# Kernel optimization log

Hardware: AMD Instinct MI355X
Metric: run time of the kernel (lower is better)

## Reference

```python
import jax, jax.numpy as jnp
import numpy as np
import math

D_MODEL = 1024
N_HEADS = 16
D_HEAD = D_MODEL // N_HEADS
DECAY_MAX = 0.99  # buggy torch init: only the LAST head's decay rate survives the loop
LN_EPS = 1e-5


def setup_inputs() -> dict:
    key = jax.random.key(0)
    ks = jax.random.split(key, 12)
    B, S = 2, 2048
    x = jax.random.normal(ks[0], (B, S, D_MODEL), dtype=jnp.float32)
    def w(k):
        return jax.random.normal(k, (D_MODEL, D_MODEL), dtype=jnp.float32) * 0.02
    return {
        "x": x,
        "Wq": w(ks[1]), "bq": jnp.zeros((D_MODEL,), jnp.float32),
        "Wk": w(ks[2]), "bk": jnp.zeros((D_MODEL,), jnp.float32),
        "Wv": w(ks[3]), "bv": jnp.zeros((D_MODEL,), jnp.float32),
        "Wg": w(ks[4]), "bg": jnp.zeros((D_MODEL,), jnp.float32),
        "Wo": w(ks[5]), "bo": jnp.zeros((D_MODEL,), jnp.float32),
        "gamma": jnp.ones((D_MODEL,), jnp.float32),
        "beta": jnp.zeros((D_MODEL,), jnp.float32),
    }


def _decay_mask(S):
    # faithful to torch buffer: decay_matrix[i,j] = DECAY_MAX**(i-j) for j<=i else 0
    i = jnp.arange(S, dtype=jnp.float32)[:, None]
    j = jnp.arange(S, dtype=jnp.float32)[None, :]
    diff = i - j
    return jnp.where(diff >= 0, jnp.power(jnp.float32(DECAY_MAX), diff), 0.0)  # [S,S]


def reference(x, Wq, bq, Wk, bk, Wv, bv, Wg, bg, Wo, bo, gamma, beta):
    B, S, D = x.shape
    H, DH = N_HEADS, D_HEAD
    # projections -> [B,H,S,DH]
    Q = (x @ Wq + bq).reshape(B, S, H, DH).transpose(0, 2, 1, 3)
    K = (x @ Wk + bk).reshape(B, S, H, DH).transpose(0, 2, 1, 3)
    V = (x @ Wv + bv).reshape(B, S, H, DH).transpose(0, 2, 1, 3)
    scores = jnp.einsum('bhsd,bhtd->bhst', Q, K) / math.sqrt(DH)  # [B,H,S,S]
    mask = _decay_mask(S)  # [S,S], broadcast over B,H (head-independent per torch bug)
    retained = jnp.einsum('bhst,bhtd->bhsd', scores * mask, V)
    retained = retained.transpose(0, 2, 1, 3).reshape(B, S, D)
    # LayerNorm over last dim
    mu = jnp.mean(retained, axis=-1, keepdims=True)
    var = jnp.var(retained, axis=-1, keepdims=True)
    normed = (retained - mu) * jax.lax.rsqrt(var + LN_EPS) * gamma + beta
    G = jax.nn.sigmoid(x @ Wg + bg)
    return (normed * G) @ Wo + bo  # dropout = identity (eval)
```

## Files before the change

### kernel.cpp

```cpp
#include <hip/hip_runtime.h>

typedef __attribute__((ext_vector_type(4))) float f32x4;
typedef __attribute__((ext_vector_type(8))) short bf16x8;
typedef unsigned short USHORT;

static __device__ __forceinline__ float bf2f(USHORT u) {
    return __uint_as_float(((unsigned)u) << 16);
}
static __device__ __forceinline__ USHORT f2bf(float f) {
    unsigned u = __float_as_uint(f);
    unsigned r = u + 0x7FFF + ((u >> 16) & 1);
    return (USHORT)(r >> 16);
}

#define GLDS16(gp, lp) __builtin_amdgcn_global_load_lds(                      \
    (const __attribute__((address_space(1))) unsigned int*)(gp),              \
    (__attribute__((address_space(3))) unsigned int*)(lp), 16, 0, 0)

__global__ __launch_bounds__(256) void k_cast_x(const float* __restrict__ x,
                                                USHORT* __restrict__ xb) {
    const int i = (blockIdx.x * 256 + threadIdx.x) * 4;
    float4 v = *(const float4*)&x[i];
    *(ushort4*)&xb[i] = make_ushort4(f2bf(v.x), f2bf(v.y), f2bf(v.z), f2bf(v.w));
}

struct TWArgs { const float* src[5]; USHORT* dst[5]; };

__global__ __launch_bounds__(256) void k_transpose_w(TWArgs ta) {
    const float* __restrict__ W  = ta.src[blockIdx.z];
    USHORT* __restrict__      WT = ta.dst[blockIdx.z];
    __shared__ USHORT t[64][65];
    const int k0 = blockIdx.y * 64, n0 = blockIdx.x * 64;
    const int tid = threadIdx.x;
#pragma unroll
    for (int s = 0; s < 4; s++) {
        int slot = tid + s * 256;
        int row = slot >> 4, c4 = (slot & 15) * 4;
        float4 vv = *(const float4*)&W[(size_t)(k0 + row) * 1024 + n0 + c4];
        t[row][c4 + 0] = f2bf(vv.x);
        t[row][c4 + 1] = f2bf(vv.y);
        t[row][c4 + 2] = f2bf(vv.z);
        t[row][c4 + 3] = f2bf(vv.w);
    }
    __syncthreads();
#pragma unroll
    for (int s = 0; s < 2; s++) {
        int slot = tid + s * 256;
        int n = slot >> 3, c8 = (slot & 7) * 8;
        USHORT tmp[8];
#pragma unroll
        for (int u = 0; u < 8; u++) tmp[u] = t[c8 + u][n];
        *(int4*)&WT[(size_t)(n0 + n) * 1024 + k0 + c8] = *(int4*)tmp;
    }
}

struct GArgs {
    const USHORT* A;
    const USHORT* W[4];
    const float*  bias[4];
    void*         dst[4];
    USHORT*       dstv;
    float         scale[4];
    int           mode[4];
};

__global__ __launch_bounds__(256, 2) void k_gemm(GArgs ga) {
    const int z = blockIdx.z;
    const USHORT* __restrict__ A  = ga.A;
    const USHORT* __restrict__ BT = ga.W[z];
    __shared__ USHORT As[128 * 32];
    __shared__ USHORT Bs[128 * 32];
    const int tid = threadIdx.x;
    const int m0 = blockIdx.y * 128, n0 = blockIdx.x * 128;
    const int w = tid >> 6, l = tid & 63, lr = l & 15, q = l >> 4;
    const int wr = w >> 1, wc = w & 1;
    const int srow = tid >> 2, sco = (tid & 3) * 8;
    f32x4 acc[4][4] = {};
    for (int k0 = 0; k0 < 1024; k0 += 32) {
        __syncthreads();
        GLDS16(&A [(size_t)(m0 + srow)      * 1024 + k0 + sco], &As[srow * 32 + sco]);
        GLDS16(&A [(size_t)(m0 + srow + 64) * 1024 + k0 + sco], &As[(srow + 64) * 32 + sco]);
        GLDS16(&BT[(size_t)(n0 + srow)      * 1024 + k0 + sco], &Bs[srow * 32 + sco]);
        GLDS16(&BT[(size_t)(n0 + srow + 64) * 1024 + k0 + sco], &Bs[(srow + 64) * 32 + sco]);
        __syncthreads();
        bf16x8 af[4], bfr[4];
#pragma unroll
        for (int mi = 0; mi < 4; mi++)
            af[mi] = *(const bf16x8*)&As[(wr * 64 + mi * 16 + lr) * 32 + q * 8];
#pragma unroll
        for (int ni = 0; ni < 4; ni++)
            bfr[ni] = *(const bf16x8*)&Bs[(wc * 64 + ni * 16 + lr) * 32 + q * 8];
#pragma unroll
        for (int mi = 0; mi < 4; mi++)
#pragma unroll
            for (int ni = 0; ni < 4; ni++)
                acc[mi][ni] = __builtin_amdgcn_mfma_f32_16x16x32_bf16(
                    af[mi], bfr[ni], acc[mi][ni], 0, 0, 0);
    }
    const float scale = ga.scale[z];
    const int mode = ga.mode[z];
    const float* __restrict__ bias = ga.bias[z];
#pragma unroll
    for (int ni = 0; ni < 4; ni++) {
        int col = n0 + wc * 64 + ni * 16 + lr;
        float bv = bias[col];
#pragma unroll
        for (int mi = 0; mi < 4; mi++) {
            int r0 = m0 + wr * 64 + mi * 16 + q * 4;
            float vr[4];
#pragma unroll
            for (int r = 0; r < 4; r++) {
                float v = acc[mi][ni][r] + bv;
                if (mode == 1) v = 1.0f / (1.0f + __expf(-v));
                vr[r] = v * scale;
            }
            if (mode == 3) {
                float* df = (float*)ga.dst[z];
#pragma unroll
                for (int r = 0; r < 4; r++)
                    df[(size_t)(r0 + r) * 1024 + col] = vr[r];
            } else if (mode == 2) {
                int b = r0 >> 11, s = r0 & 2047;
                int h = col >> 6, d = col & 63;
                const float NP1 = 1.0101010101010102f;
                float c0 = exp2f(0.014499569695115089f * (float)(s & 63));
                float c1 = c0 * NP1, c2 = c1 * NP1, c3 = c2 * NP1;
                *(ushort4*)&ga.dstv[(size_t)(((b * 16 + h) * 64) + d) * 2048 + s] =
                    make_ushort4(f2bf(vr[0] * c0), f2bf(vr[1] * c1),
                                 f2bf(vr[2] * c2), f2bf(vr[3] * c3));
            } else {
                USHORT* db = (USHORT*)ga.dst[z];
#pragma unroll
                for (int r = 0; r < 4; r++)
                    db[(size_t)(r0 + r) * 1024 + col] = f2bf(vr[r]);
            }
        }
    }
}

__global__ __launch_bounds__(256, 2) void k_attn(const USHORT* __restrict__ Q,
                                                 const USHORT* __restrict__ K,
                                                 const USHORT* __restrict__ VT,
                                                 float* __restrict__ R) {
    const int bh = blockIdx.x;
    const int b = bh >> 4, h = bh & 15;
    const int rr = blockIdx.y;
    const int iblk = (rr < 8) ? rr : 23 - rr;
    const int i0 = iblk * 128;
    const int tid = threadIdx.x, w = tid >> 6, l = tid & 63, lr = l & 15, q = l >> 4;
    __shared__ USHORT Qs[128 * 72];
    __shared__ USHORT Ks[64 * 72];
    __shared__ USHORT Vs[64 * 72];
    __shared__ USHORT Ps[4][32 * 72];
    const float L2D = -0.014499569695115089f;
    const float C16 = 0.8514577710948755f;
#pragma unroll
    for (int s = 0; s < 4; s++) {
        int slot = tid + s * 256;
        int rw = slot >> 3, c8 = (slot & 7) * 8;
        *(int4*)&Qs[rw * 72 + c8] =
            *(const int4*)&Q[(size_t)(b * 2048 + i0 + rw) * 1024 + h * 64 + c8];
    }
    const int iw0 = i0 + w * 32;
    f32x4 accr[4][2] = {};
    const int njb = 2 * iblk + 2;
    for (int jb = 0; jb < njb; jb++) {
        const int j0 = jb * 64;
        {
            int r0_ = tid >> 3, c0 = (tid & 7) * 8;
            int slot1 = tid + 256;
            int r1_ = slot1 >> 3, c1 = (slot1 & 7) * 8;
            int4 kv0 = *(const int4*)&K[(size_t)(b * 2048 + j0 + r0_) * 1024 + h * 64 + c0];
            int4 kv1 = *(const int4*)&K[(size_t)(b * 2048 + j0 + r1_) * 1024 + h * 64 + c1];
            int4 vv0 = *(const int4*)&VT[(size_t)(bh * 64 + r0_) * 2048 + j0 + c0];
            int4 vv1 = *(const int4*)&VT[(size_t)(bh * 64 + r1_) * 2048 + j0 + c1];
            __syncthreads();
            *(int4*)&Ks[r0_ * 72 + c0] = kv0;
            *(int4*)&Ks[r1_ * 72 + c1] = kv1;
            *(int4*)&Vs[r0_ * 72 + c0] = vv0;
            *(int4*)&Vs[r1_ * 72 + c1] = vv1;
            __syncthreads();
        }
        if (j0 <= iw0 + 31) {
            f32x4 accp[4][2] = {};
#pragma unroll
            for (int kk = 0; kk < 2; kk++) {
                bf16x8 bqf[2];
#pragma unroll
                for (int it = 0; it < 2; it++)
                    bqf[it] = *(const bf16x8*)&Qs[(w * 32 + it * 16 + lr) * 72 + kk * 32 + q * 8];
#pragma unroll
                for (int jt = 0; jt < 4; jt++) {
                    bf16x8 akf = *(const bf16x8*)&Ks[(jt * 16 + lr) * 72 + kk * 32 + q * 8];
#pragma unroll
                    for (int it = 0; it < 2; it++)
                        accp[jt][it] = __builtin_amdgcn_mfma_f32_16x16x32_bf16(
                            akf, bqf[it], accp[jt][it], 0, 0, 0);
                }
            }
            const float fb = exp2f(L2D * (float)(iw0 - j0 + lr));
            const float F[2] = { fb, fb * C16 };
            const bool partial = (j0 + 63 > iw0);
#pragma unroll
            for (int jt = 0; jt < 4; jt++) {
#pragma unroll
                for (int it = 0; it < 2; it++) {
                    float v0 = accp[jt][it][0] * F[it];
                    float v1 = accp[jt][it][1] * F[it];
                    float v2 = accp[jt][it][2] * F[it];
                    float v3 = accp[jt][it][3] * F[it];
                    if (partial) {
                        const int ii = iw0 + it * 16 + lr;
                        const int jj = j0 + jt * 16 + q * 4;
                        if (jj + 0 > ii) v0 = 0.0f;
                        if (jj + 1 > ii) v1 = 0.0f;
                        if (jj + 2 > ii) v2 = 0.0f;
                        if (jj + 3 > ii) v3 = 0.0f;
                    }
                    unsigned w0 = __builtin_amdgcn_perm(
                        __float_as_uint(v1), __float_as_uint(v0), 0x07060302u);
                    unsigned w1 = __builtin_amdgcn_perm(
                        __float_as_uint(v3), __float_as_uint(v2), 0x07060302u);
                    *(uint2*)&Ps[w][(it * 16 + lr) * 72 + jt * 16 + q * 4] =
                        make_uint2(w0, w1);
                }
            }
            asm volatile("s_waitcnt lgkmcnt(0)" ::: "memory");
#pragma unroll
            for (int kk = 0; kk < 2; kk++) {
                bf16x8 bpf[2];
#pragma unroll
                for (int it = 0; it < 2; it++)
                    bpf[it] = *(const bf16x8*)&Ps[w][(it * 16 + lr) * 72 + kk * 32 + q * 8];
#pragma unroll
                for (int dt = 0; dt < 4; dt++) {
                    bf16x8 avf = *(const bf16x8*)&Vs[(dt * 16 + lr) * 72 + kk * 32 + q * 8];
#pragma unroll
                    for (int it = 0; it < 2; it++)
                        accr[dt][it] = __builtin_amdgcn_mfma_f32_16x16x32_bf16(
                            avf, bpf[it], accr[dt][it], 0, 0, 0);
                }
            }
        }
    }
#pragma unroll
    for (int it = 0; it < 2; it++) {
        int i = i0 + w * 32 + it * 16 + lr;
#pragma unroll
        for (int dt = 0; dt < 4; dt++) {
            *(f32x4*)&R[(size_t)(b * 2048 + i) * 1024 + h * 64 + dt * 16 + q * 4] =
                accr[dt][it];
        }
    }
}

__global__ __launch_bounds__(256) void k_ln_gate(const float* __restrict__ R,
                                                 const USHORT* __restrict__ G,
                                                 const float* __restrict__ gamma,
                                                 const float* __restrict__ beta,
                                                 USHORT* __restrict__ NG) {
    const int row = blockIdx.x, tid = threadIdx.x;
    const float4 v = *(const float4*)&R[(size_t)row * 1024 + tid * 4];
    float vv[4] = { v.x, v.y, v.z, v.w };
    float s  = vv[0] + vv[1] + vv[2] + vv[3];
    float s2 = vv[0]*vv[0] + vv[1]*vv[1] + vv[2]*vv[2] + vv[3]*vv[3];
#pragma unroll
    for (int o = 32; o > 0; o >>= 1) {
        s  += __shfl_down(s, o, 64);
        s2 += __shfl_down(s2, o, 64);
    }
    __shared__ float red[8];
    if ((tid & 63) == 0) { red[tid >> 6] = s; red[4 + (tid >> 6)] = s2; }
    __syncthreads();
    const float ts  = red[0] + red[1] + red[2] + red[3];
    const float ts2 = red[4] + red[5] + red[6] + red[7];
    const float mu  = ts * (1.0f / 1024.0f);
    const float var = ts2 * (1.0f / 1024.0f) - mu * mu;
    const float inv = rsqrtf(var + 1e-5f);
    ushort4 g4 = *(const ushort4*)&G[(size_t)row * 1024 + tid * 4];
    float4 gm = *(const float4*)&gamma[tid * 4];
    float4 bt = *(const float4*)&beta[tid * 4];
    USHORT gg[4]  = { g4.x, g4.y, g4.z, g4.w };
    float  gmm[4] = { gm.x, gm.y, gm.z, gm.w };
    float  btt[4] = { bt.x, bt.y, bt.z, bt.w };
    USHORT o4[4];
#pragma unroll
    for (int u = 0; u < 4; u++) {
        float nv = (vv[u] - mu) * inv * gmm[u] + btt[u];
        o4[u] = f2bf(nv * bf2f(gg[u]));
    }
    *(ushort4*)&NG[(size_t)row * 1024 + tid * 4] = make_ushort4(o4[0], o4[1], o4[2], o4[3]);
}

extern "C" void kernel_launch(void* const* d_in, const int* in_sizes, int n_in,
                              void* d_out, int out_size, void* d_ws, size_t ws_size,
                              hipStream_t stream) {
    const float* x     = (const float*)d_in[0];
    const float* Wq    = (const float*)d_in[1];
    const float* bq    = (const float*)d_in[2];
    const float* Wk    = (const float*)d_in[3];
    const float* bk    = (const float*)d_in[4];
    const float* Wv    = (const float*)d_in[5];
    const float* bv    = (const float*)d_in[6];
    const float* Wg    = (const float*)d_in[7];
    const float* bg    = (const float*)d_in[8];
    const float* Wo    = (const float*)d_in[9];
    const float* bo    = (const float*)d_in[10];
    const float* gamma = (const float*)d_in[11];
    const float* beta  = (const float*)d_in[12];

    char* ws = (char*)d_ws;
    const size_t MB = 1 << 20;
    USHORT* WqT = (USHORT*)(ws + 0 * MB);
    USHORT* WkT = (USHORT*)(ws + 2 * MB);
    USHORT* WvT = (USHORT*)(ws + 4 * MB);
    USHORT* WgT = (USHORT*)(ws + 6 * MB);
    USHORT* WoT = (USHORT*)(ws + 8 * MB);
    USHORT* Qb  = (USHORT*)(ws + 10 * MB);
    USHORT* Kb  = (USHORT*)(ws + 18 * MB);
    USHORT* VTb = (USHORT*)(ws + 26 * MB);
    USHORT* Gb  = (USHORT*)(ws + 34 * MB);
    USHORT* NGb = Qb;
    USHORT* Xb  = (USHORT*)d_out;
    float*  Rf  = (float*)d_out;

    k_cast_x<<<4096, 256, 0, stream>>>(x, Xb);
    {
        TWArgs ta;
        ta.src[0] = Wq; ta.src[1] = Wk; ta.src[2] = Wv; ta.src[3] = Wg; ta.src[4] = Wo;
        ta.dst[0] = WqT; ta.dst[1] = WkT; ta.dst[2] = WvT; ta.dst[3] = WgT; ta.dst[4] = WoT;
        k_transpose_w<<<dim3(16, 16, 5), 256, 0, stream>>>(ta);
    }
    {
        GArgs ga;
        ga.A = Xb;
        ga.W[0] = WqT; ga.W[1] = WkT; ga.W[2] = WvT; ga.W[3] = WgT;
        ga.bias[0] = bq; ga.bias[1] = bk; ga.bias[2] = bv; ga.bias[3] = bg;
        ga.dst[0] = Qb; ga.dst[1] = Kb; ga.dst[2] = nullptr; ga.dst[3] = Gb;
        ga.dstv = VTb;
        ga.scale[0] = 0.125f; ga.scale[1] = 1.0f; ga.scale[2] = 1.0f; ga.scale[3] = 1.0f;
        ga.mode[0] = 0; ga.mode[1] = 0; ga.mode[2] = 2; ga.mode[3] = 1;
        k_gemm<<<dim3(8, 32, 4), 256, 0, stream>>>(ga);
    }
    k_attn<<<dim3(32, 16), 256, 0, stream>>>(Qb, Kb, VTb, Rf);
    k_ln_gate<<<4096, 256, 0, stream>>>(Rf, Gb, gamma, beta, NGb);
    {
        GArgs go;
        go.A = NGb;
        for (int i = 0; i < 4; i++) {
            go.W[i] = WoT; go.bias[i] = bo; go.dst[i] = d_out;
            go.scale[i] = 1.0f; go.mode[i] = 3;
        }
        go.dstv = nullptr;
        k_gemm<<<dim3(8, 32, 1), 256, 0, stream>>>(go);
    }
}
```

Baseline: 233.6 us.

## Double-buffer LDS tiles in GEMM and attention kernels to overlap loads

The GEMM kernel now holds two LDS buffers for the A/B tiles and issues global-to-LDS loads for the next k-step before computing on the current one, so each iteration needs one barrier instead of two. The attention kernel likewise double-buffers its K/V tiles: it prefetches the next block into registers before computing and writes them into the alternate LDS buffer after compute. The aim is to hide global memory latency behind MFMA work. The cost is doubled LDS use for these tiles, which can lower occupancy, plus extra live registers in attention.

```diff
diff --git a/kernel.cpp b/kernel.cpp
--- a/kernel.cpp
+++ b/kernel.cpp
@@ -16,6 +16,9 @@
 #define GLDS16(gp, lp) __builtin_amdgcn_global_load_lds(                      \
     (const __attribute__((address_space(1))) unsigned int*)(gp),              \
     (__attribute__((address_space(3))) unsigned int*)(lp), 16, 0, 0)
+
+#define LGKM_BARRIER() asm volatile("s_waitcnt lgkmcnt(0)\ns_barrier" ::: "memory")
+#define FULL_BARRIER() asm volatile("s_waitcnt vmcnt(0) lgkmcnt(0)\ns_barrier" ::: "memory")
 
 __global__ __launch_bounds__(256) void k_cast_x(const float* __restrict__ x,
                                                 USHORT* __restrict__ xb) {
@@ -68,28 +71,36 @@
     const int z = blockIdx.z;
     const USHORT* __restrict__ A  = ga.A;
     const USHORT* __restrict__ BT = ga.W[z];
-    __shared__ USHORT As[128 * 32];
-    __shared__ USHORT Bs[128 * 32];
+    __shared__ USHORT As[2][128 * 32];
+    __shared__ USHORT Bs[2][128 * 32];
     const int tid = threadIdx.x;
     const int m0 = blockIdx.y * 128, n0 = blockIdx.x * 128;
     const int w = tid >> 6, l = tid & 63, lr = l & 15, q = l >> 4;
     const int wr = w >> 1, wc = w & 1;
     const int srow = tid >> 2, sco = (tid & 3) * 8;
     f32x4 acc[4][4] = {};
-    for (int k0 = 0; k0 < 1024; k0 += 32) {
-        __syncthreads();
-        GLDS16(&A [(size_t)(m0 + srow)      * 1024 + k0 + sco], &As[srow * 32 + sco]);
-        GLDS16(&A [(size_t)(m0 + srow + 64) * 1024 + k0 + sco], &As[(srow + 64) * 32 + sco]);
-        GLDS16(&BT[(size_t)(n0 + srow)      * 1024 + k0 + sco], &Bs[srow * 32 + sco]);
-        GLDS16(&BT[(size_t)(n0 + srow + 64) * 1024 + k0 + sco], &Bs[(srow + 64) * 32 + sco]);
-        __syncthreads();
+    GLDS16(&A [(size_t)(m0 + srow)      * 1024 + sco], &As[0][srow * 32 + sco]);
+    GLDS16(&A [(size_t)(m0 + srow + 64) * 1024 + sco], &As[0][(srow + 64) * 32 + sco]);
+    GLDS16(&BT[(size_t)(n0 + srow)      * 1024 + sco], &Bs[0][srow * 32 + sco]);
+    GLDS16(&BT[(size_t)(n0 + srow + 64) * 1024 + sco], &Bs[0][(srow + 64) * 32 + sco]);
+    for (int kt = 0; kt < 32; kt++) {
+        const int cur = kt & 1;
+        FULL_BARRIER();
+        if (kt + 1 < 32) {
+            const int k1 = (kt + 1) * 32;
+            const int nxt = 1 - cur;
+            GLDS16(&A [(size_t)(m0 + srow)      * 1024 + k1 + sco], &As[nxt][srow * 32 + sco]);
+            GLDS16(&A [(size_t)(m0 + srow + 64) * 1024 + k1 + sco], &As[nxt][(srow + 64) * 32 + sco]);
+            GLDS16(&BT[(size_t)(n0 + srow)      * 1024 + k1 + sco], &Bs[nxt][srow * 32 + sco]);
+            GLDS16(&BT[(size_t)(n0 + srow + 64) * 1024 + k1 + sco], &Bs[nxt][(srow + 64) * 32 + sco]);
+        }
         bf16x8 af[4], bfr[4];
 #pragma unroll
         for (int mi = 0; mi < 4; mi++)
-            af[mi] = *(const bf16x8*)&As[(wr * 64 + mi * 16 + lr) * 32 + q * 8];
+            af[mi] = *(const bf16x8*)&As[cur][(wr * 64 + mi * 16 + lr) * 32 + q * 8];
 #pragma unroll
         for (int ni = 0; ni < 4; ni++)
-            bfr[ni] = *(const bf16x8*)&Bs[(wc * 64 + ni * 16 + lr) * 32 + q * 8];
+            bfr[ni] = *(const bf16x8*)&Bs[cur][(wc * 64 + ni * 16 + lr) * 32 + q * 8];
 #pragma unroll
         for (int mi = 0; mi < 4; mi++)
 #pragma unroll
@@ -149,8 +160,8 @@
     const int i0 = iblk * 128;
     const int tid = threadIdx.x, w = tid >> 6, l = tid & 63, lr = l & 15, q = l >> 4;
     __shared__ USHORT Qs[128 * 72];
-    __shared__ USHORT Ks[64 * 72];
-    __shared__ USHORT Vs[64 * 72];
+    __shared__ USHORT Ks[2][64 * 72];
+    __shared__ USHORT Vs[2][64 * 72];
     __shared__ USHORT Ps[4][32 * 72];
     const float L2D = -0.014499569695115089f;
     const float C16 = 0.8514577710948755f;
@@ -162,25 +173,29 @@
             *(const int4*)&Q[(size_t)(b * 2048 + i0 + rw) * 1024 + h * 64 + c8];
     }
     const int iw0 = i0 + w * 32;
+    const int r0_ = tid >> 3, c0 = (tid & 7) * 8;
+    const int njb = 2 * iblk + 2;
+    int4 kv0, kv1, vv0, vv1;
+    kv0 = *(const int4*)&K [(size_t)(b * 2048 + r0_)      * 1024 + h * 64 + c0];
+    kv1 = *(const int4*)&K [(size_t)(b * 2048 + r0_ + 32) * 1024 + h * 64 + c0];
+    vv0 = *(const int4*)&VT[(size_t)(bh * 64 + r0_)      * 2048 + c0];
+    vv1 = *(const int4*)&VT[(size_t)(bh * 64 + r0_ + 32) * 2048 + c0];
+    *(int4*)&Ks[0][r0_ * 72 + c0]        = kv0;
+    *(int4*)&Ks[0][(r0_ + 32) * 72 + c0] = kv1;
+    *(int4*)&Vs[0][r0_ * 72 + c0]        = vv0;
+    *(int4*)&Vs[0][(r0_ + 32) * 72 + c0] = vv1;
     f32x4 accr[4][2] = {};
-    const int njb = 2 * iblk + 2;
     for (int jb = 0; jb < njb; jb++) {
         const int j0 = jb * 64;
-        {
-            int r0_ = tid >> 3, c0 = (tid & 7) * 8;
-            int slot1 = tid + 256;
-            int r1_ = slot1 >> 3, c1 = (slot1 & 7) * 8;
-            int4 kv0 = *(const int4*)&K[(size_t)(b * 2048 + j0 + r0_) * 1024 + h * 64 + c0];
-            int4 kv1 = *(const int4*)&K[(size_t)(b * 2048 + j0 + r1_) * 1024 + h * 64 + c1];
-            int4 vv0 = *(const int4*)&VT[(size_t)(bh * 64 + r0_) * 2048 + j0 + c0];
-            int4 vv1 = *(const int4*)&VT[(size_t)(bh * 64 + r1_) * 2048 + j0 + c1];
-            __syncthreads();
-            *(int4*)&Ks[r0_ * 72 + c0] = kv0;
-            *(int4*)&Ks[r1_ * 72 + c1] = kv1;
-            *(int4*)&Vs[r0_ * 72 + c0] = vv0;
-            *(int4*)&Vs[r1_ * 72 + c1] = vv1;
-            __syncthreads();
-        }
+        const int cur = jb & 1;
+        if (jb + 1 < njb) {
+            const int j1 = j0 + 64;
+            kv0 = *(const int4*)&K [(size_t)(b * 2048 + j1 + r0_)      * 1024 + h * 64 + c0];
+            kv1 = *(const int4*)&K [(size_t)(b * 2048 + j1 + r0_ + 32) * 1024 + h * 64 + c0];
+            vv0 = *(const int4*)&VT[(size_t)(bh * 64 + r0_)      * 2048 + j1 + c0];
+            vv1 = *(const int4*)&VT[(size_t)(bh * 64 + r0_ + 32) * 2048 + j1 + c0];
+        }
+        LGKM_BARRIER();
         if (j0 <= iw0 + 31) {
             f32x4 accp[4][2] = {};
 #pragma unroll
@@ -191,7 +206,7 @@
                     bqf[it] = *(const bf16x8*)&Qs[(w * 32 + it * 16 + lr) * 72 + kk * 32 + q * 8];
 #pragma unroll
                 for (int jt = 0; jt < 4; jt++) {
-                    bf16x8 akf = *(const bf16x8*)&Ks[(jt * 16 + lr) * 72 + kk * 32 + q * 8];
+                    bf16x8 akf = *(const bf16x8*)&Ks[cur][(jt * 16 + lr) * 72 + kk * 32 + q * 8];
 #pragma unroll
                     for (int it = 0; it < 2; it++)
                         accp[jt][it] = __builtin_amdgcn_mfma_f32_16x16x32_bf16(
@@ -234,13 +249,20 @@
                     bpf[it] = *(const bf16x8*)&Ps[w][(it * 16 + lr) * 72 + kk * 32 + q * 8];
 #pragma unroll
                 for (int dt = 0; dt < 4; dt++) {
-                    bf16x8 avf = *(const bf16x8*)&Vs[(dt * 16 + lr) * 72 + kk * 32 + q * 8];
+                    bf16x8 avf = *(const bf16x8*)&Vs[cur][(dt * 16 + lr) * 72 + kk * 32 + q * 8];
 #pragma unroll
                     for (int it = 0; it < 2; it++)
                         accr[dt][it] = __builtin_amdgcn_mfma_f32_16x16x32_bf16(
                             avf, bpf[it], accr[dt][it], 0, 0, 0);
                 }
             }
+        }
+        if (jb + 1 < njb) {
+            const int nxt = 1 - cur;
+            *(int4*)&Ks[nxt][r0_ * 72 + c0]        = kv0;
+            *(int4*)&Ks[nxt][(r0_ + 32) * 72 + c0] = kv1;
+            *(int4*)&Vs[nxt][r0_ * 72 + c0]        = vv0;
+            *(int4*)&Vs[nxt][(r0_ + 32) * 72 + c0] = vv1;
         }
     }
 #pragma unroll
```

Result: faster. 225.9 us (-3.3%).

## Replace quadratic decay attention with chunked recurrent form and fuse LayerNorm into output GEMM

Applied to the files above, without the earlier changes.

The full masked S×S attention is replaced with a chunkwise retention formulation. One kernel computes a per-64-row chunk V^T K state, and an apply kernel combines a decayed prefix sum of those states with the intra-chunk causal attention, using a hi/lo bf16 split to keep precision. LayerNorm row statistics are accumulated with atomics in the apply kernel, and normalization plus gating are fused into the A-tile staging of the output GEMM, which removes the separate LN kernel and the fp32 R round trip. The GEMM gains LDS double buffering, and the x cast and weight transpose are merged into one prep launch. In exchange the apply kernel does a serial O(c) prefix reduction over chunk states, and the LN path adds float atomics plus extra per-tile ALU work in the output GEMM.

```diff
diff --git a/kernel.cpp b/kernel.cpp
--- a/kernel.cpp
+++ b/kernel.cpp
@@ -17,45 +17,61 @@
     (const __attribute__((address_space(1))) unsigned int*)(gp),              \
     (__attribute__((address_space(3))) unsigned int*)(lp), 16, 0, 0)
 
-__global__ __launch_bounds__(256) void k_cast_x(const float* __restrict__ x,
-                                                USHORT* __restrict__ xb) {
-    const int i = (blockIdx.x * 256 + threadIdx.x) * 4;
-    float4 v = *(const float4*)&x[i];
-    *(ushort4*)&xb[i] = make_ushort4(f2bf(v.x), f2bf(v.y), f2bf(v.z), f2bf(v.w));
-}
-
-struct TWArgs { const float* src[5]; USHORT* dst[5]; };
-
-__global__ __launch_bounds__(256) void k_transpose_w(TWArgs ta) {
-    const float* __restrict__ W  = ta.src[blockIdx.z];
-    USHORT* __restrict__      WT = ta.dst[blockIdx.z];
+#define FULL_BARRIER() asm volatile("s_waitcnt vmcnt(0) lgkmcnt(0)\ns_barrier" ::: "memory")
+
+#define D64 0.52559648f
+#define L2D (-0.014499569695115089f)
+
+struct PrepArgs { const float* src[5]; USHORT* dst[5]; const float* x; USHORT* xb; };
+
+__global__ __launch_bounds__(256) void k_prep(PrepArgs pa) {
+    const int z = blockIdx.z;
+    const int tid = threadIdx.x;
     __shared__ USHORT t[64][65];
-    const int k0 = blockIdx.y * 64, n0 = blockIdx.x * 64;
-    const int tid = threadIdx.x;
-#pragma unroll
-    for (int s = 0; s < 4; s++) {
-        int slot = tid + s * 256;
-        int row = slot >> 4, c4 = (slot & 15) * 4;
-        float4 vv = *(const float4*)&W[(size_t)(k0 + row) * 1024 + n0 + c4];
-        t[row][c4 + 0] = f2bf(vv.x);
-        t[row][c4 + 1] = f2bf(vv.y);
-        t[row][c4 + 2] = f2bf(vv.z);
-        t[row][c4 + 3] = f2bf(vv.w);
-    }
-    __syncthreads();
-#pragma unroll
-    for (int s = 0; s < 2; s++) {
-        int slot = tid + s * 256;
-        int n = slot >> 3, c8 = (slot & 7) * 8;
-        USHORT tmp[8];
-#pragma unroll
-        for (int u = 0; u < 8; u++) tmp[u] = t[c8 + u][n];
-        *(int4*)&WT[(size_t)(n0 + n) * 1024 + k0 + c8] = *(int4*)tmp;
+    if (z < 5) {
+        const float* __restrict__ W  = pa.src[z];
+        USHORT* __restrict__      WT = pa.dst[z];
+        const int k0 = blockIdx.y * 64, n0 = blockIdx.x * 64;
+#pragma unroll
+        for (int s = 0; s < 4; s++) {
+            int slot = tid + s * 256;
+            int row = slot >> 4, c4 = (slot & 15) * 4;
+            float4 vv = *(const float4*)&W[(size_t)(k0 + row) * 1024 + n0 + c4];
+            t[row][c4 + 0] = f2bf(vv.x);
+            t[row][c4 + 1] = f2bf(vv.y);
+            t[row][c4 + 2] = f2bf(vv.z);
+            t[row][c4 + 3] = f2bf(vv.w);
+        }
+        __syncthreads();
+#pragma unroll
+        for (int s = 0; s < 2; s++) {
+            int slot = tid + s * 256;
+            int n = slot >> 3, c8 = (slot & 7) * 8;
+            USHORT tmp[8];
+#pragma unroll
+            for (int u = 0; u < 8; u++) tmp[u] = t[c8 + u][n];
+            *(int4*)&WT[(size_t)(n0 + n) * 1024 + k0 + c8] = *(int4*)tmp;
+        }
+    } else {
+        const int bi = blockIdx.y * 16 + blockIdx.x;
+        const float* xs = pa.x + (size_t)bi * 16384;
+        USHORT* xd = pa.xb + (size_t)bi * 16384;
+#pragma unroll
+        for (int u = 0; u < 16; u++) {
+            int idx = u * 1024 + tid * 4;
+            float4 v = *(const float4*)&xs[idx];
+            *(ushort4*)&xd[idx] = make_ushort4(f2bf(v.x), f2bf(v.y), f2bf(v.z), f2bf(v.w));
+        }
     }
 }
 
 struct GArgs {
     const USHORT* A;
+    const USHORT* G;
+    const float*  gamma;
+    const float*  beta;
+    const float*  stats;
+    int           ln;
     const USHORT* W[4];
     const float*  bias[4];
     void*         dst[4];
@@ -66,30 +82,70 @@
 
 __global__ __launch_bounds__(256, 2) void k_gemm(GArgs ga) {
     const int z = blockIdx.z;
-    const USHORT* __restrict__ A  = ga.A;
     const USHORT* __restrict__ BT = ga.W[z];
-    __shared__ USHORT As[128 * 32];
-    __shared__ USHORT Bs[128 * 32];
+    __shared__ USHORT As[2][128 * 32];
+    __shared__ USHORT Bs[2][128 * 32];
     const int tid = threadIdx.x;
     const int m0 = blockIdx.y * 128, n0 = blockIdx.x * 128;
     const int w = tid >> 6, l = tid & 63, lr = l & 15, q = l >> 4;
     const int wr = w >> 1, wc = w & 1;
     const int srow = tid >> 2, sco = (tid & 3) * 8;
     f32x4 acc[4][4] = {};
-    for (int k0 = 0; k0 < 1024; k0 += 32) {
-        __syncthreads();
-        GLDS16(&A [(size_t)(m0 + srow)      * 1024 + k0 + sco], &As[srow * 32 + sco]);
-        GLDS16(&A [(size_t)(m0 + srow + 64) * 1024 + k0 + sco], &As[(srow + 64) * 32 + sco]);
-        GLDS16(&BT[(size_t)(n0 + srow)      * 1024 + k0 + sco], &Bs[srow * 32 + sco]);
-        GLDS16(&BT[(size_t)(n0 + srow + 64) * 1024 + k0 + sco], &Bs[(srow + 64) * 32 + sco]);
-        __syncthreads();
+    float mu0 = 0.f, iv0 = 0.f, mu1 = 0.f, iv1 = 0.f;
+    if (ga.ln) {
+        float2 s0 = *(const float2*)&ga.stats[(m0 + srow) * 2];
+        mu0 = s0.x * (1.0f / 1024.0f);
+        iv0 = rsqrtf(fmaxf(s0.y * (1.0f / 1024.0f) - mu0 * mu0, 0.0f) + 1e-5f);
+        float2 s1 = *(const float2*)&ga.stats[(m0 + srow + 64) * 2];
+        mu1 = s1.x * (1.0f / 1024.0f);
+        iv1 = rsqrtf(fmaxf(s1.y * (1.0f / 1024.0f) - mu1 * mu1, 0.0f) + 1e-5f);
+    }
+#define STAGE_A(kt_, buf_)                                                       \
+    do {                                                                         \
+        const int kk0 = (kt_) * 32;                                              \
+        if (ga.ln) {                                                             \
+            float4 g0 = *(const float4*)&ga.gamma[kk0 + sco];                    \
+            float4 g1 = *(const float4*)&ga.gamma[kk0 + sco + 4];                \
+            float4 b0 = *(const float4*)&ga.beta[kk0 + sco];                     \
+            float4 b1 = *(const float4*)&ga.beta[kk0 + sco + 4];                 \
+            float gmv[8] = {g0.x,g0.y,g0.z,g0.w,g1.x,g1.y,g1.z,g1.w};            \
+            float btv[8] = {b0.x,b0.y,b0.z,b0.w,b1.x,b1.y,b1.z,b1.w};            \
+            _Pragma("unroll")                                                    \
+            for (int hrow = 0; hrow < 2; hrow++) {                               \
+                float mu = hrow ? mu1 : mu0, iv = hrow ? iv1 : iv0;              \
+                size_t off = (size_t)(m0 + srow + hrow * 64) * 1024 + kk0 + sco; \
+                USHORT r8[8], g8[8], a8[8];                                      \
+                *(int4*)r8 = *(const int4*)&ga.A[off];                           \
+                *(int4*)g8 = *(const int4*)&ga.G[off];                           \
+                _Pragma("unroll")                                                \
+                for (int u = 0; u < 8; u++)                                      \
+                    a8[u] = f2bf(((bf2f(r8[u]) - mu) * iv * gmv[u] + btv[u])     \
+                                 * bf2f(g8[u]));                                 \
+                *(int4*)&As[buf_][(srow + hrow * 64) * 32 + sco] = *(int4*)a8;   \
+            }                                                                    \
+        } else {                                                                 \
+            GLDS16(&ga.A[(size_t)(m0 + srow) * 1024 + kk0 + sco],                \
+                   &As[buf_][srow * 32 + sco]);                                  \
+            GLDS16(&ga.A[(size_t)(m0 + srow + 64) * 1024 + kk0 + sco],           \
+                   &As[buf_][(srow + 64) * 32 + sco]);                           \
+        }                                                                        \
+        GLDS16(&BT[(size_t)(n0 + srow) * 1024 + kk0 + sco],                      \
+               &Bs[buf_][srow * 32 + sco]);                                      \
+        GLDS16(&BT[(size_t)(n0 + srow + 64) * 1024 + kk0 + sco],                 \
+               &Bs[buf_][(srow + 64) * 32 + sco]);                               \
+    } while (0)
+    STAGE_A(0, 0);
+    for (int kt = 0; kt < 32; kt++) {
+        const int cur = kt & 1;
+        FULL_BARRIER();
+        if (kt + 1 < 32) STAGE_A(kt + 1, 1 - cur);
         bf16x8 af[4], bfr[4];
 #pragma unroll
         for (int mi = 0; mi < 4; mi++)
-            af[mi] = *(const bf16x8*)&As[(wr * 64 + mi * 16 + lr) * 32 + q * 8];
+            af[mi] = *(const bf16x8*)&As[cur][(wr * 64 + mi * 16 + lr) * 32 + q * 8];
 #pragma unroll
         for (int ni = 0; ni < 4; ni++)
-            bfr[ni] = *(const bf16x8*)&Bs[(wc * 64 + ni * 16 + lr) * 32 + q * 8];
+            bfr[ni] = *(const bf16x8*)&Bs[cur][(wc * 64 + ni * 16 + lr) * 32 + q * 8];
 #pragma unroll
         for (int mi = 0; mi < 4; mi++)
 #pragma unroll
@@ -97,6 +153,7 @@
                 acc[mi][ni] = __builtin_amdgcn_mfma_f32_16x16x32_bf16(
                     af[mi], bfr[ni], acc[mi][ni], 0, 0, 0);
     }
+#undef STAGE_A
     const float scale = ga.scale[z];
     const int mode = ga.mode[z];
     const float* __restrict__ bias = ga.bias[z];
@@ -113,6 +170,13 @@
                 float v = acc[mi][ni][r] + bv;
                 if (mode == 1) v = 1.0f / (1.0f + __expf(-v));
                 vr[r] = v * scale;
+            }
+            if (mode == 4) {
+                float d0 = exp2f(L2D * (float)(r0 & 63));
+                vr[0] *= d0;
+                vr[1] *= d0 * 0.99f;
+                vr[2] *= d0 * 0.9801f;
+                vr[3] *= d0 * 0.970299f;
             }
             if (mode == 3) {
                 float* df = (float*)ga.dst[z];
@@ -123,7 +187,7 @@
                 int b = r0 >> 11, s = r0 & 2047;
                 int h = col >> 6, d = col & 63;
                 const float NP1 = 1.0101010101010102f;
-                float c0 = exp2f(0.014499569695115089f * (float)(s & 63));
+                float c0 = exp2f(-L2D * (float)(s & 63));
                 float c1 = c0 * NP1, c2 = c1 * NP1, c3 = c2 * NP1;
                 *(ushort4*)&ga.dstv[(size_t)(((b * 16 + h) * 64) + d) * 2048 + s] =
                     make_ushort4(f2bf(vr[0] * c0), f2bf(vr[1] * c1),
@@ -138,158 +202,178 @@
     }
 }
 
-__global__ __launch_bounds__(256, 2) void k_attn(const USHORT* __restrict__ Q,
-                                                 const USHORT* __restrict__ K,
-                                                 const USHORT* __restrict__ VT,
-                                                 float* __restrict__ R) {
-    const int bh = blockIdx.x;
+__global__ __launch_bounds__(256) void k_attn_u(const USHORT* __restrict__ K,
+                                                const USHORT* __restrict__ VT,
+                                                float* __restrict__ U) {
+    const int bh = blockIdx.x, c = blockIdx.y;
     const int b = bh >> 4, h = bh & 15;
-    const int rr = blockIdx.y;
-    const int iblk = (rr < 8) ? rr : 23 - rr;
-    const int i0 = iblk * 128;
     const int tid = threadIdx.x, w = tid >> 6, l = tid & 63, lr = l & 15, q = l >> 4;
-    __shared__ USHORT Qs[128 * 72];
+    __shared__ USHORT KT[64 * 72];
+    __shared__ USHORT Vs[64 * 72];
+#pragma unroll
+    for (int s = 0; s < 2; s++) {
+        int slot = tid + s * 256;
+        int row = slot >> 3, co = (slot & 7) * 8;
+        USHORT kv[8];
+        *(int4*)kv = *(const int4*)&K[(size_t)(b * 2048 + c * 64 + row) * 1024 + h * 64 + co];
+#pragma unroll
+        for (int u = 0; u < 8; u++) KT[(co + u) * 72 + row] = kv[u];
+        *(int4*)&Vs[row * 72 + co] =
+            *(const int4*)&VT[(size_t)(bh * 64 + row) * 2048 + c * 64 + co];
+    }
+    __syncthreads();
+    f32x4 acc[4] = {};
+    bf16x8 av[2];
+#pragma unroll
+    for (int kk = 0; kk < 2; kk++)
+        av[kk] = *(const bf16x8*)&Vs[(w * 16 + lr) * 72 + kk * 32 + q * 8];
+#pragma unroll
+    for (int dkt = 0; dkt < 4; dkt++)
+#pragma unroll
+        for (int kk = 0; kk < 2; kk++) {
+            bf16x8 bk = *(const bf16x8*)&KT[(dkt * 16 + lr) * 72 + kk * 32 + q * 8];
+            acc[dkt] = __builtin_amdgcn_mfma_f32_16x16x32_bf16(av[kk], bk, acc[dkt], 0, 0, 0);
+        }
+    float* slot = U + (size_t)(bh * 32 + c) * 4096;
+#pragma unroll
+    for (int dkt = 0; dkt < 4; dkt++)
+#pragma unroll
+        for (int r = 0; r < 4; r++)
+            slot[(w * 16 + q * 4 + r) * 64 + dkt * 16 + lr] = acc[dkt][r] * D64;
+}
+
+__global__ __launch_bounds__(256, 2) void k_apply(const USHORT* __restrict__ Q,
+                                                  const USHORT* __restrict__ K,
+                                                  const USHORT* __restrict__ VT,
+                                                  const float* __restrict__ U,
+                                                  USHORT* __restrict__ R,
+                                                  float* __restrict__ stats) {
+    const int bh = blockIdx.x, c = blockIdx.y;
+    const int b = bh >> 4, h = bh & 15;
+    const int i0 = c * 64;
+    const int tid = threadIdx.x, w = tid >> 6, l = tid & 63, lr = l & 15, q = l >> 4;
+    __shared__ USHORT Qs[64 * 72];
     __shared__ USHORT Ks[64 * 72];
     __shared__ USHORT Vs[64 * 72];
-    __shared__ USHORT Ps[4][32 * 72];
-    const float L2D = -0.014499569695115089f;
-    const float C16 = 0.8514577710948755f;
-#pragma unroll
-    for (int s = 0; s < 4; s++) {
+    __shared__ USHORT Ps[4][16 * 72];
+    __shared__ unsigned Spk[4096];
+#pragma unroll
+    for (int s = 0; s < 2; s++) {
         int slot = tid + s * 256;
-        int rw = slot >> 3, c8 = (slot & 7) * 8;
-        *(int4*)&Qs[rw * 72 + c8] =
-            *(const int4*)&Q[(size_t)(b * 2048 + i0 + rw) * 1024 + h * 64 + c8];
-    }
-    const int iw0 = i0 + w * 32;
-    f32x4 accr[4][2] = {};
-    const int njb = 2 * iblk + 2;
-    for (int jb = 0; jb < njb; jb++) {
-        const int j0 = jb * 64;
-        {
-            int r0_ = tid >> 3, c0 = (tid & 7) * 8;
-            int slot1 = tid + 256;
-            int r1_ = slot1 >> 3, c1 = (slot1 & 7) * 8;
-            int4 kv0 = *(const int4*)&K[(size_t)(b * 2048 + j0 + r0_) * 1024 + h * 64 + c0];
-            int4 kv1 = *(const int4*)&K[(size_t)(b * 2048 + j0 + r1_) * 1024 + h * 64 + c1];
-            int4 vv0 = *(const int4*)&VT[(size_t)(bh * 64 + r0_) * 2048 + j0 + c0];
-            int4 vv1 = *(const int4*)&VT[(size_t)(bh * 64 + r1_) * 2048 + j0 + c1];
-            __syncthreads();
-            *(int4*)&Ks[r0_ * 72 + c0] = kv0;
-            *(int4*)&Ks[r1_ * 72 + c1] = kv1;
-            *(int4*)&Vs[r0_ * 72 + c0] = vv0;
-            *(int4*)&Vs[r1_ * 72 + c1] = vv1;
-            __syncthreads();
-        }
-        if (j0 <= iw0 + 31) {
-            f32x4 accp[4][2] = {};
+        int row = slot >> 3, c8 = (slot & 7) * 8;
+        *(int4*)&Qs[row * 72 + c8] =
+            *(const int4*)&Q[(size_t)(b * 2048 + i0 + row) * 1024 + h * 64 + c8];
+        *(int4*)&Ks[row * 72 + c8] =
+            *(const int4*)&K[(size_t)(b * 2048 + i0 + row) * 1024 + h * 64 + c8];
+        *(int4*)&Vs[row * 72 + c8] =
+            *(const int4*)&VT[(size_t)(bh * 64 + row) * 2048 + i0 + c8];
+    }
+    if (c > 0) {
+        float sa[16] = {};
+        const float* Ub = U + (size_t)bh * 32 * 4096 + tid * 16;
+        for (int cp = 0; cp < c; cp++) {
+            const float* p = Ub + (size_t)cp * 4096;
+#pragma unroll
+            for (int u4 = 0; u4 < 4; u4++) {
+                float4 uv = *(const float4*)(p + u4 * 4);
+                sa[u4 * 4 + 0] = sa[u4 * 4 + 0] * D64 + uv.x;
+                sa[u4 * 4 + 1] = sa[u4 * 4 + 1] * D64 + uv.y;
+                sa[u4 * 4 + 2] = sa[u4 * 4 + 2] * D64 + uv.z;
+                sa[u4 * 4 + 3] = sa[u4 * 4 + 3] * D64 + uv.w;
+            }
+        }
+#pragma unroll
+        for (int u = 0; u < 16; u++) {
+            USHORT hi = f2bf(sa[u]);
+            float  lo = sa[u] - bf2f(hi);
+            Spk[tid * 16 + u] = (unsigned)hi | ((unsigned)f2bf(lo) << 16);
+        }
+    }
+    __syncthreads();
+    bf16x8 bqf[2];
+#pragma unroll
+    for (int kk = 0; kk < 2; kk++)
+        bqf[kk] = *(const bf16x8*)&Qs[(w * 16 + lr) * 72 + kk * 32 + q * 8];
+    f32x4 accr[4] = {};
+    if (c > 0) {
+#pragma unroll
+        for (int dt = 0; dt < 4; dt++)
 #pragma unroll
             for (int kk = 0; kk < 2; kk++) {
-                bf16x8 bqf[2];
-#pragma unroll
-                for (int it = 0; it < 2; it++)
-                    bqf[it] = *(const bf16x8*)&Qs[(w * 32 + it * 16 + lr) * 72 + kk * 32 + q * 8];
-#pragma unroll
-                for (int jt = 0; jt < 4; jt++) {
-                    bf16x8 akf = *(const bf16x8*)&Ks[(jt * 16 + lr) * 72 + kk * 32 + q * 8];
-#pragma unroll
-                    for (int it = 0; it < 2; it++)
-                        accp[jt][it] = __builtin_amdgcn_mfma_f32_16x16x32_bf16(
-                            akf, bqf[it], accp[jt][it], 0, 0, 0);
+                const unsigned* sp = &Spk[(dt * 16 + lr) * 64 + kk * 32 + q * 8];
+                uint4 pa = *(const uint4*)sp;
+                uint4 pb = *(const uint4*)(sp + 4);
+                unsigned pk[8] = { pa.x, pa.y, pa.z, pa.w, pb.x, pb.y, pb.z, pb.w };
+                bf16x8 hi, lo;
+#pragma unroll
+                for (int u = 0; u < 8; u++) {
+                    hi[u] = (short)(pk[u] & 0xffffu);
+                    lo[u] = (short)(pk[u] >> 16);
                 }
-            }
-            const float fb = exp2f(L2D * (float)(iw0 - j0 + lr));
-            const float F[2] = { fb, fb * C16 };
-            const bool partial = (j0 + 63 > iw0);
+                accr[dt] = __builtin_amdgcn_mfma_f32_16x16x32_bf16(hi, bqf[kk], accr[dt], 0, 0, 0);
+                accr[dt] = __builtin_amdgcn_mfma_f32_16x16x32_bf16(lo, bqf[kk], accr[dt], 0, 0, 0);
+            }
+    }
+    {
+        f32x4 accp[4] = {};
+#pragma unroll
+        for (int kk = 0; kk < 2; kk++)
 #pragma unroll
             for (int jt = 0; jt < 4; jt++) {
-#pragma unroll
-                for (int it = 0; it < 2; it++) {
-                    float v0 = accp[jt][it][0] * F[it];
-                    float v1 = accp[jt][it][1] * F[it];
-                    float v2 = accp[jt][it][2] * F[it];
-                    float v3 = accp[jt][it][3] * F[it];
-                    if (partial) {
-                        const int ii = iw0 + it * 16 + lr;
-                        const int jj = j0 + jt * 16 + q * 4;
-                        if (jj + 0 > ii) v0 = 0.0f;
-                        if (jj + 1 > ii) v1 = 0.0f;
-                        if (jj + 2 > ii) v2 = 0.0f;
-                        if (jj + 3 > ii) v3 = 0.0f;
-                    }
-                    unsigned w0 = __builtin_amdgcn_perm(
-                        __float_as_uint(v1), __float_as_uint(v0), 0x07060302u);
-                    unsigned w1 = __builtin_amdgcn_perm(
-                        __float_as_uint(v3), __float_as_uint(v2), 0x07060302u);
-                    *(uint2*)&Ps[w][(it * 16 + lr) * 72 + jt * 16 + q * 4] =
-                        make_uint2(w0, w1);
-                }
-            }
-            asm volatile("s_waitcnt lgkmcnt(0)" ::: "memory");
-#pragma unroll
-            for (int kk = 0; kk < 2; kk++) {
-                bf16x8 bpf[2];
-#pragma unroll
-                for (int it = 0; it < 2; it++)
-                    bpf[it] = *(const bf16x8*)&Ps[w][(it * 16 + lr) * 72 + kk * 32 + q * 8];
-#pragma unroll
-                for (int dt = 0; dt < 4; dt++) {
-                    bf16x8 avf = *(const bf16x8*)&Vs[(dt * 16 + lr) * 72 + kk * 32 + q * 8];
-#pragma unroll
-                    for (int it = 0; it < 2; it++)
-                        accr[dt][it] = __builtin_amdgcn_mfma_f32_16x16x32_bf16(
-                            avf, bpf[it], accr[dt][it], 0, 0, 0);
-                }
-            }
-        }
-    }
-#pragma unroll
-    for (int it = 0; it < 2; it++) {
-        int i = i0 + w * 32 + it * 16 + lr;
+                bf16x8 akf = *(const bf16x8*)&Ks[(jt * 16 + lr) * 72 + kk * 32 + q * 8];
+                accp[jt] = __builtin_amdgcn_mfma_f32_16x16x32_bf16(akf, bqf[kk], accp[jt], 0, 0, 0);
+            }
+        const int ii = w * 16 + lr;
+#pragma unroll
+        for (int jt = 0; jt < 4; jt++) {
+            const int jj = jt * 16 + q * 4;
+            float v0 = (jj + 0 <= ii) ? accp[jt][0] : 0.0f;
+            float v1 = (jj + 1 <= ii) ? accp[jt][1] : 0.0f;
+            float v2 = (jj + 2 <= ii) ? accp[jt][2] : 0.0f;
+            float v3 = (jj + 3 <= ii) ? accp[jt][3] : 0.0f;
+            unsigned w0 = __builtin_amdgcn_perm(
+                __float_as_uint(v1), __float_as_uint(v0), 0x07060302u);
+            unsigned w1 = __builtin_amdgcn_perm(
+                __float_as_uint(v3), __float_as_uint(v2), 0x07060302u);
+            *(uint2*)&Ps[w][lr * 72 + jt * 16 + q * 4] = make_uint2(w0, w1);
+        }
+        asm volatile("s_waitcnt lgkmcnt(0)" ::: "memory");
+#pragma unroll
+        for (int kk = 0; kk < 2; kk++) {
+            bf16x8 bpf = *(const bf16x8*)&Ps[w][lr * 72 + kk * 32 + q * 8];
+#pragma unroll
+            for (int dt = 0; dt < 4; dt++) {
+                bf16x8 avf = *(const bf16x8*)&Vs[(dt * 16 + lr) * 72 + kk * 32 + q * 8];
+                accr[dt] = __builtin_amdgcn_mfma_f32_16x16x32_bf16(avf, bpf, accr[dt], 0, 0, 0);
+            }
+        }
+    }
+    {
+        float s1 = 0.f, s2 = 0.f;
+#pragma unroll
+        for (int dt = 0; dt < 4; dt++)
+#pragma unroll
+            for (int r = 0; r < 4; r++) {
+                float v = accr[dt][r];
+                s1 += v; s2 += v * v;
+            }
+        s1 += __shfl_down(s1, 32); s2 += __shfl_down(s2, 32);
+        s1 += __shfl_down(s1, 16); s2 += __shfl_down(s2, 16);
+        if (q == 0) {
+            int row = b * 2048 + i0 + w * 16 + lr;
+            atomicAdd(&stats[row * 2 + 0], s1);
+            atomicAdd(&stats[row * 2 + 1], s2);
+        }
+    }
+    {
+        const int i = i0 + w * 16 + lr;
 #pragma unroll
         for (int dt = 0; dt < 4; dt++) {
-            *(f32x4*)&R[(size_t)(b * 2048 + i) * 1024 + h * 64 + dt * 16 + q * 4] =
-                accr[dt][it];
-        }
-    }
-}
-
-__global__ __launch_bounds__(256) void k_ln_gate(const float* __restrict__ R,
-                                                 const USHORT* __restrict__ G,
-                                                 const float* __restrict__ gamma,
-                                                 const float* __restrict__ beta,
-                                                 USHORT* __restrict__ NG) {
-    const int row = blockIdx.x, tid = threadIdx.x;
-    const float4 v = *(const float4*)&R[(size_t)row * 1024 + tid * 4];
-    float vv[4] = { v.x, v.y, v.z, v.w };
-    float s  = vv[0] + vv[1] + vv[2] + vv[3];
-    float s2 = vv[0]*vv[0] + vv[1]*vv[1] + vv[2]*vv[2] + vv[3]*vv[3];
-#pragma unroll
-    for (int o = 32; o > 0; o >>= 1) {
-        s  += __shfl_down(s, o, 64);
-        s2 += __shfl_down(s2, o, 64);
-    }
-    __shared__ float red[8];
-    if ((tid & 63) == 0) { red[tid >> 6] = s; red[4 + (tid >> 6)] = s2; }
-    __syncthreads();
-    const float ts  = red[0] + red[1] + red[2] + red[3];
-    const float ts2 = red[4] + red[5] + red[6] + red[7];
-    const float mu  = ts * (1.0f / 1024.0f);
-    const float var = ts2 * (1.0f / 1024.0f) - mu * mu;
-    const float inv = rsqrtf(var + 1e-5f);
-    ushort4 g4 = *(const ushort4*)&G[(size_t)row * 1024 + tid * 4];
-    float4 gm = *(const float4*)&gamma[tid * 4];
-    float4 bt = *(const float4*)&beta[tid * 4];
-    USHORT gg[4]  = { g4.x, g4.y, g4.z, g4.w };
-    float  gmm[4] = { gm.x, gm.y, gm.z, gm.w };
-    float  btt[4] = { bt.x, bt.y, bt.z, bt.w };
-    USHORT o4[4];
-#pragma unroll
-    for (int u = 0; u < 4; u++) {
-        float nv = (vv[u] - mu) * inv * gmm[u] + btt[u];
-        o4[u] = f2bf(nv * bf2f(gg[u]));
-    }
-    *(ushort4*)&NG[(size_t)row * 1024 + tid * 4] = make_ushort4(o4[0], o4[1], o4[2], o4[3]);
+            f32x4 a = accr[dt];
+            *(ushort4*)&R[(size_t)(b * 2048 + i) * 1024 + h * 64 + dt * 16 + q * 4] =
+                make_ushort4(f2bf(a[0]), f2bf(a[1]), f2bf(a[2]), f2bf(a[3]));
+        }
+    }
 }
 
 extern "C" void kernel_launch(void* const* d_in, const int* in_sizes, int n_in,
@@ -320,33 +404,36 @@
     USHORT* Kb  = (USHORT*)(ws + 18 * MB);
     USHORT* VTb = (USHORT*)(ws + 26 * MB);
     USHORT* Gb  = (USHORT*)(ws + 34 * MB);
-    USHORT* NGb = Qb;
+    float*  Sts = (float*) (ws + 42 * MB);
     USHORT* Xb  = (USHORT*)d_out;
-    float*  Rf  = (float*)d_out;
-
-    k_cast_x<<<4096, 256, 0, stream>>>(x, Xb);
-    {
-        TWArgs ta;
-        ta.src[0] = Wq; ta.src[1] = Wk; ta.src[2] = Wv; ta.src[3] = Wg; ta.src[4] = Wo;
-        ta.dst[0] = WqT; ta.dst[1] = WkT; ta.dst[2] = WvT; ta.dst[3] = WgT; ta.dst[4] = WoT;
-        k_transpose_w<<<dim3(16, 16, 5), 256, 0, stream>>>(ta);
-    }
+    float*  Ust = (float*)d_out;
+
+    {
+        PrepArgs pa;
+        pa.src[0] = Wq; pa.src[1] = Wk; pa.src[2] = Wv; pa.src[3] = Wg; pa.src[4] = Wo;
+        pa.dst[0] = WqT; pa.dst[1] = WkT; pa.dst[2] = WvT; pa.dst[3] = WgT; pa.dst[4] = WoT;
+        pa.x = x; pa.xb = Xb;
+        k_prep<<<dim3(16, 16, 6), 256, 0, stream>>>(pa);
+    }
+    hipMemsetAsync((void*)Sts, 0, 4096 * 2 * sizeof(float), stream);
     {
         GArgs ga;
-        ga.A = Xb;
+        ga.A = Xb; ga.G = nullptr; ga.gamma = gamma; ga.beta = beta;
+        ga.stats = Sts; ga.ln = 0;
         ga.W[0] = WqT; ga.W[1] = WkT; ga.W[2] = WvT; ga.W[3] = WgT;
         ga.bias[0] = bq; ga.bias[1] = bk; ga.bias[2] = bv; ga.bias[3] = bg;
         ga.dst[0] = Qb; ga.dst[1] = Kb; ga.dst[2] = nullptr; ga.dst[3] = Gb;
         ga.dstv = VTb;
         ga.scale[0] = 0.125f; ga.scale[1] = 1.0f; ga.scale[2] = 1.0f; ga.scale[3] = 1.0f;
-        ga.mode[0] = 0; ga.mode[1] = 0; ga.mode[2] = 2; ga.mode[3] = 1;
+        ga.mode[0] = 4; ga.mode[1] = 0; ga.mode[2] = 2; ga.mode[3] = 1;
         k_gemm<<<dim3(8, 32, 4), 256, 0, stream>>>(ga);
     }
-    k_attn<<<dim3(32, 16), 256, 0, stream>>>(Qb, Kb, VTb, Rf);
-    k_ln_gate<<<4096, 256, 0, stream>>>(Rf, Gb, gamma, beta, NGb);
+    k_attn_u<<<dim3(32, 32), 256, 0, stream>>>(Kb, VTb, Ust);
+    k_apply<<<dim3(32, 32), 256, 0, stream>>>(Qb, Kb, VTb, Ust, Kb, Sts);
     {
         GArgs go;
-        go.A = NGb;
+        go.A = Kb;
+        go.G = Gb; go.gamma = gamma; go.beta = beta; go.stats = Sts; go.ln = 1;
         for (int i = 0; i < 4; i++) {
             go.W[i] = WoT; go.bias[i] = bo; go.dst[i] = d_out;
             go.scale[i] = 1.0f; go.mode[i] = 3;
```

After: 252.6 us. 1.08x slower.
